# Kernel tuning notes

Measured on AMD Instinct MI355X. Metric: run time of the kernel, lower is better.

## Reference

```python
import jax, jax.numpy as jnp
import numpy as np

NEIGHBORS = 16  # init kwarg 'neighbors'


def _mlp(x, params):
    # SetTransform with reduction='none': pointwise MLP, ReLU between layers, linear output
    for W, b in params[:-1]:
        x = jax.nn.relu(x @ W + b)
    W, b = params[-1]
    return x @ W + b


def setup_inputs() -> dict:
    key = jax.random.key(0)
    B, K, P, DIM, C_IN = 4, 2048, 4096, 3, 64
    C_MID, C_OUT = 32, 128
    WH = 32          # weight_hidden sizes
    FH = 256         # final_hidden size
    FIN = C_IN * C_MID  # 2048, final_conv input

    ks = jax.random.split(key, 16)

    def lin(k, fan_in, fan_out):
        k1, k2 = jax.random.split(k)
        s = 1.0 / np.sqrt(fan_in)
        W = jax.random.uniform(k1, (fan_in, fan_out), minval=-s, maxval=s, dtype=jnp.float32)
        b = jax.random.uniform(k2, (fan_out,), minval=-s, maxval=s, dtype=jnp.float32)
        return W, b

    wc0_W, wc0_b = lin(ks[0], DIM, WH)
    wc1_W, wc1_b = lin(ks[1], WH, WH)
    wc2_W, wc2_b = lin(ks[2], WH, C_MID)
    fc0_W, fc0_b = lin(ks[3], FIN, FH)
    fc1_W, fc1_b = lin(ks[4], FH, C_OUT)

    return {
        "keys": jax.random.normal(ks[5], (B, K, DIM), dtype=jnp.float32),
        "points": jax.random.normal(ks[6], (B, P, DIM), dtype=jnp.float32),
        "feats": jax.random.normal(ks[7], (B, P, C_IN), dtype=jnp.float32),
        "wc0_W": wc0_W, "wc0_b": wc0_b,
        "wc1_W": wc1_W, "wc1_b": wc1_b,
        "wc2_W": wc2_W, "wc2_b": wc2_b,
        "fc0_W": fc0_W, "fc0_b": fc0_b,
        "fc1_W": fc1_W, "fc1_b": fc1_b,
    }


def reference(keys, points, feats,
              wc0_W, wc0_b, wc1_W, wc1_b, wc2_W, wc2_b,
              fc0_W, fc0_b, fc1_W, fc1_b):
    B, K, _ = keys.shape
    # Euclidean dist_fn: rel_pos [B,K,P,dim], squared dist [B,K,P]; all points valid
    dist_vec = points[:, None, :, :] - keys[:, :, None, :]
    dist = jnp.sum(dist_vec * dist_vec, axis=-1)
    # k smallest distances -> neighbor indices [B,K,N]
    _, idxs = jax.lax.top_k(-dist, NEIGHBORS)
    # gather relative positions [B,K,N,dim] and neighbor features [B,K,N,c_in]
    neighbor_rel = jnp.take_along_axis(dist_vec, idxs[..., None], axis=2)
    b_idx = jnp.arange(B)[:, None, None]
    neighbor_feats = feats[b_idx, idxs]
    # per-edge weight MLP: [B,K,N,dim] -> [B,K,N,c_mid]
    m = _mlp(neighbor_rel, [(wc0_W, wc0_b), (wc1_W, wc1_b), (wc2_W, wc2_b)])
    # masked matmul aggregation (all neighbors valid under euclidean dist_fn):
    # m^T @ neighbor_feats -> [B,K,c_mid,c_in], flattened to [B,K,c_mid*c_in]
    e = jnp.einsum('bknm,bknc->bkmc', m, neighbor_feats).reshape(B, K, -1)
    # final pointwise MLP -> [B,K,c_out]
    return _mlp(e, [(fc0_W, fc0_b), (fc1_W, fc1_b)])
```

## Files before the change

### kernel.cpp

```cpp
#include <hip/hip_runtime.h>
#include <cfloat>
#include <climits>

#define BATCH 4
#define KQ    2048
#define NP    4096
#define CIN   64
#define CMID  32
#define NB    16
#define NBINS 4096
#define CANDCAP 256
#define QPB   8

typedef short   bf16x8  __attribute__((ext_vector_type(8)));
typedef float   floatx4 __attribute__((ext_vector_type(4)));

__device__ __forceinline__ unsigned short f2bf(float f) {
  unsigned u = __float_as_uint(f);
  u = (u + 0x7fffu + ((u >> 16) & 1u)) >> 16;
  return (unsigned short)u;
}
__device__ __forceinline__ float bf2f(unsigned short u) {
  return __uint_as_float((unsigned)u << 16);
}

__device__ __forceinline__ void load_lds16(const void* g, void* l) {
  __builtin_amdgcn_global_load_lds(
      (const __attribute__((address_space(1))) unsigned int*)g,
      (__attribute__((address_space(3))) unsigned int*)l, 16, 0, 0);
}

__global__ __launch_bounds__(256) void select_topk(
    const float* __restrict__ keys, const float* __restrict__ points,
    int* __restrict__ nidx_g) {
  __shared__ __align__(16) int hist[NBINS];
  __shared__ int   psum[256];
  __shared__ float cand_d[CANDCAP];
  __shared__ int   cand_i[CANDCAP];
  __shared__ int   nidx[NB];
  __shared__ int   sel_cnt, cand_cnt, sBin, sCbelow;

  const int tid = threadIdx.x;
  const int b   = blockIdx.x >> 11;

#pragma unroll
  for (int t = 0; t < 4; ++t)
    *reinterpret_cast<int4*>(&hist[(tid + t * 256) * 4]) = int4{0, 0, 0, 0};
  if (tid == 0) { sel_cnt = 0; cand_cnt = 0; }

  const float kx = keys[blockIdx.x * 3 + 0];
  const float ky = keys[blockIdx.x * 3 + 1];
  const float kz = keys[blockIdx.x * 3 + 2];
  __syncthreads();

  const float4* pv =
      reinterpret_cast<const float4*>(points + (size_t)b * NP * 3) + (size_t)tid * 12;
  float f[48];
#pragma unroll
  for (int c = 0; c < 12; ++c) {
    const float4 v = pv[c];
    f[c * 4 + 0] = v.x; f[c * 4 + 1] = v.y; f[c * 4 + 2] = v.z; f[c * 4 + 3] = v.w;
  }
  float dreg[16];
#pragma unroll
  for (int j = 0; j < 16; ++j) {
    const float dx = f[j * 3 + 0] - kx;
    const float dy = f[j * 3 + 1] - ky;
    const float dz = f[j * 3 + 2] - kz;
    const float d  = dx * dx + dy * dy + dz * dz;
    dreg[j] = d;
    atomicAdd(&hist[__float_as_uint(d) >> 19], 1);
  }
  __syncthreads();

  {
    const int base = tid * 16;
    int s = 0;
#pragma unroll
    for (int t = 0; t < 4; ++t) {
      const int4 hv = *reinterpret_cast<const int4*>(&hist[base + t * 4]);
      s += hv.x + hv.y + hv.z + hv.w;
    }
    psum[tid] = s;
  }
  __syncthreads();

  if (tid < 64) {
    const int q = psum[tid * 4] + psum[tid * 4 + 1] + psum[tid * 4 + 2] + psum[tid * 4 + 3];
    int incl = q;
#pragma unroll
    for (int off = 1; off < 64; off <<= 1) {
      int u = __shfl_up(incl, off);
      if (tid >= off) incl += u;
    }
    unsigned long long bal = __ballot(incl >= NB);
    int firstlane = __ffsll((long long)bal) - 1;
    if (tid == firstlane) {
      int cum = incl - q;
      int bin = -1;
      for (int t = 0; t < 4 && bin < 0; ++t) {
        const int ps = psum[tid * 4 + t];
        if (cum + ps >= NB) {
          const int b0 = (tid * 4 + t) * 16;
          for (int j = 0; j < 16; ++j) {
            const int h = hist[b0 + j];
            if (cum + h >= NB) { bin = b0 + j; break; }
            cum += h;
          }
        } else cum += ps;
      }
      sBin = bin; sCbelow = cum;
    }
  }
  __syncthreads();

  const unsigned B = (unsigned)sBin;
#pragma unroll
  for (int j = 0; j < 16; ++j) {
    const int i = tid * 16 + j;
    const unsigned bk = __float_as_uint(dreg[j]) >> 19;
    if (bk < B) {
      int pos = atomicAdd(&sel_cnt, 1);
      nidx[pos] = i;
    } else if (bk == B) {
      int pos = atomicAdd(&cand_cnt, 1);
      if (pos < CANDCAP) { cand_d[pos] = dreg[j]; cand_i[pos] = i; }
    }
  }
  __syncthreads();

  {
    const int rem = NB - sCbelow;
    const int cc  = min(cand_cnt, CANDCAP);
    for (int j = tid; j < cc; j += 256) {
      const float dj = cand_d[j]; const int ij = cand_i[j];
      int rank = 0;
      for (int k = 0; k < cc; ++k) {
        const float dk = cand_d[k]; const int ik = cand_i[k];
        rank += (dk < dj || (dk == dj && ik < ij)) ? 1 : 0;
      }
      if (rank < rem) nidx[sCbelow + rank] = ij;
    }
  }
  __syncthreads();

  if (tid < NB) nidx_g[blockIdx.x * NB + tid] = nidx[tid];
}

__global__ __launch_bounds__(256) void edge_prep(
    const float* __restrict__ keys, const float* __restrict__ points,
    const float* __restrict__ feats, const int* __restrict__ nidx_g,
    const float* __restrict__ wc0_W, const float* __restrict__ wc0_b,
    const float* __restrict__ wc1_W, const float* __restrict__ wc1_b,
    const float* __restrict__ wc2_W, const float* __restrict__ wc2_b,
    const float* __restrict__ fc0_W, const float* __restrict__ fc1_W,
    unsigned short* __restrict__ W0T, unsigned short* __restrict__ W1T,
    unsigned short* __restrict__ E) {
  __shared__ __align__(16) float w0[96], b0v[32], w1[1024], b1v[32], w2[1024], b2v[32];
  __shared__ int   idx_s[QPB * NB];
  __shared__ __align__(16) unsigned short m_bf[QPB * NB][40];
  __shared__ __align__(16) char u_mem[128 * 144];
  float (*h2_all)[36]        = reinterpret_cast<float(*)[36]>(u_mem);
  unsigned short (*f_bf)[72] = reinterpret_cast<unsigned short(*)[72]>(u_mem);
  float (*tt)[33]            = reinterpret_cast<float(*)[33]>(u_mem);

  const int tid = threadIdx.x;
  const int bid = blockIdx.x;
  const int q0  = bid * QPB;
  const int b   = q0 >> 11;

  if (bid < 544) {
    const float* W; unsigned short* WT; int K, N, k0, n0;
    if (bid < 512) { W = fc0_W; WT = W0T; K = 2048; N = 256;
                     k0 = (bid >> 3) * 32; n0 = (bid & 7) * 32; }
    else           { W = fc1_W; WT = W1T; K = 256;  N = 128;
                     k0 = ((bid - 512) >> 2) * 32; n0 = ((bid - 512) & 3) * 32; }
    const int tx = tid & 31, ty = tid >> 5;
#pragma unroll
    for (int p = 0; p < 4; ++p)
      tt[ty + p * 8][tx] = W[(size_t)(k0 + ty + p * 8) * N + n0 + tx];
    __syncthreads();
#pragma unroll
    for (int p = 0; p < 4; ++p)
      WT[(size_t)(n0 + ty + p * 8) * K + k0 + tx] = f2bf(tt[tx][ty + p * 8]);
    __syncthreads();
  }

  if (tid < 96) w0[tid] = wc0_W[tid];
  for (int i = tid; i < 1024; i += 256) { w1[i] = wc1_W[i]; w2[i] = wc2_W[i]; }
  if (tid < 32) { b0v[tid] = wc0_b[tid]; b1v[tid] = wc1_b[tid]; b2v[tid] = wc2_b[tid]; }
  if (tid < QPB * NB) idx_s[tid] = nidx_g[q0 * NB + tid];
  __syncthreads();

  const int edge = tid & 127;
  const int half = tid >> 7;
  const int ob   = half * 16;
  const int qe   = edge >> 4;
  const int idx  = idx_s[edge];
  {
    const float* p  = points + ((size_t)b * NP + idx) * 3;
    const float* kq = keys + (size_t)(q0 + qe) * 3;
    const float rx = p[0] - kq[0], ry = p[1] - kq[1], rz = p[2] - kq[2];

    float h1[32];
#pragma unroll
    for (int o4 = 0; o4 < 8; ++o4) {
      const float4 a = *reinterpret_cast<const float4*>(&w0[o4 * 4]);
      const float4 c = *reinterpret_cast<const float4*>(&w0[32 + o4 * 4]);
      const float4 d = *reinterpret_cast<const float4*>(&w0[64 + o4 * 4]);
      const float4 e = *reinterpret_cast<const float4*>(&b0v[o4 * 4]);
      h1[o4 * 4 + 0] = fmaxf(0.f, rx * a.x + ry * c.x + rz * d.x + e.x);
      h1[o4 * 4 + 1] = fmaxf(0.f, rx * a.y + ry * c.y + rz * d.y + e.y);
      h1[o4 * 4 + 2] = fmaxf(0.f, rx * a.z + ry * c.z + rz * d.z + e.z);
      h1[o4 * 4 + 3] = fmaxf(0.f, rx * a.w + ry * c.w + rz * d.w + e.w);
    }

    float acc2[16];
#pragma unroll
    for (int j = 0; j < 16; ++j) acc2[j] = b1v[ob + j];
#pragma unroll
    for (int i = 0; i < 32; ++i) {
      const float hv = h1[i];
#pragma unroll
      for (int j4 = 0; j4 < 4; ++j4) {
        const float4 w = *reinterpret_cast<const float4*>(&w1[i * 32 + ob + j4 * 4]);
        acc2[j4 * 4 + 0] += hv * w.x;
        acc2[j4 * 4 + 1] += hv * w.y;
        acc2[j4 * 4 + 2] += hv * w.z;
        acc2[j4 * 4 + 3] += hv * w.w;
      }
    }
#pragma unroll
    for (int j4 = 0; j4 < 4; ++j4) {
      float4 o4v;
      o4v.x = fmaxf(acc2[j4 * 4 + 0], 0.f);
      o4v.y = fmaxf(acc2[j4 * 4 + 1], 0.f);
      o4v.z = fmaxf(acc2[j4 * 4 + 2], 0.f);
      o4v.w = fmaxf(acc2[j4 * 4 + 3], 0.f);
      *reinterpret_cast<float4*>(&h2_all[edge][ob + j4 * 4]) = o4v;
    }
  }
  __syncthreads();

  float mo[16];
#pragma unroll
  for (int j = 0; j < 16; ++j) mo[j] = b2v[ob + j];
#pragma unroll
  for (int i = 0; i < 32; ++i) {
    const float hv = h2_all[edge][i];
#pragma unroll
    for (int j4 = 0; j4 < 4; ++j4) {
      const float4 w = *reinterpret_cast<const float4*>(&w2[i * 32 + ob + j4 * 4]);
      mo[j4 * 4 + 0] += hv * w.x;
      mo[j4 * 4 + 1] += hv * w.y;
      mo[j4 * 4 + 2] += hv * w.z;
      mo[j4 * 4 + 3] += hv * w.w;
    }
  }
#pragma unroll
  for (int j = 0; j < 8; ++j) {
    const unsigned lo = f2bf(mo[2 * j]), hi = f2bf(mo[2 * j + 1]);
    *reinterpret_cast<unsigned*>(&m_bf[edge][ob + 2 * j]) = lo | (hi << 16);
  }
  __syncthreads();

#pragma unroll
  for (int t = 0; t < 8; ++t) {
    const int task = tid + t * 256;
    const int row = task >> 4, ch = task & 15;
    const float4 v = *reinterpret_cast<const float4*>(
        feats + ((size_t)b * NP + idx_s[row]) * CIN + ch * 4);
    ushort4 o4;
    o4.x = f2bf(v.x); o4.y = f2bf(v.y); o4.z = f2bf(v.z); o4.w = f2bf(v.w);
    *reinterpret_cast<ushort4*>(&f_bf[row][ch * 4]) = o4;
  }
  __syncthreads();

  const int wv = tid >> 6, lane = tid & 63;
  const int co = lane & 7, mg = lane >> 3;
#pragma unroll
  for (int it = 0; it < 2; ++it) {
    const int q = wv + it * 4;
    float acc[4][8] = {};
#pragma unroll
    for (int n = 0; n < 16; ++n) {
      const int row = q * 16 + n;
      const ushort4 m4 = *reinterpret_cast<const ushort4*>(&m_bf[row][mg * 4]);
      const float mv[4] = {bf2f(m4.x), bf2f(m4.y), bf2f(m4.z), bf2f(m4.w)};
      const uint4 fv = *reinterpret_cast<const uint4*>(&f_bf[row][co * 8]);
      float fc[8];
      fc[0] = __uint_as_float(fv.x << 16); fc[1] = __uint_as_float(fv.x & 0xffff0000u);
      fc[2] = __uint_as_float(fv.y << 16); fc[3] = __uint_as_float(fv.y & 0xffff0000u);
      fc[4] = __uint_as_float(fv.z << 16); fc[5] = __uint_as_float(fv.z & 0xffff0000u);
      fc[6] = __uint_as_float(fv.w << 16); fc[7] = __uint_as_float(fv.w & 0xffff0000u);
#pragma unroll
      for (int i = 0; i < 4; ++i)
#pragma unroll
        for (int j = 0; j < 8; ++j) acc[i][j] += mv[i] * fc[j];
    }
    unsigned short* Eq = E + (size_t)(q0 + q) * 2048;
#pragma unroll
    for (int i = 0; i < 4; ++i) {
      const int mid = mg * 4 + i;
      uint4 o;
      o.x = (unsigned)f2bf(acc[i][0]) | ((unsigned)f2bf(acc[i][1]) << 16);
      o.y = (unsigned)f2bf(acc[i][2]) | ((unsigned)f2bf(acc[i][3]) << 16);
      o.z = (unsigned)f2bf(acc[i][4]) | ((unsigned)f2bf(acc[i][5]) << 16);
      o.w = (unsigned)f2bf(acc[i][6]) | ((unsigned)f2bf(acc[i][7]) << 16);
      *reinterpret_cast<uint4*>(&Eq[mid * 64 + co * 8]) = o;
    }
  }
}

template <int KDIM, bool RELU, bool OUTBF16, bool SWIZZLE>
__global__ __launch_bounds__(256) void gemm_mfma(
    const unsigned short* __restrict__ A,
    const unsigned short* __restrict__ Bt,
    const float* __restrict__ bias,
    void* __restrict__ Cout, int ldc) {
  __shared__ __align__(16) unsigned short Al[64 * 128];
  __shared__ __align__(16) unsigned short Bl[64 * 128];
  const int tid  = threadIdx.x;
  int m0, n0;
  if (SWIZZLE) {
    const int L    = blockIdx.x;
    const int slot = L >> 3;
    m0 = ((L & 7) * 16 + (slot >> 2)) * 64;
    n0 = (slot & 3) * 64;
  } else {
    m0 = blockIdx.x * 64;
    n0 = blockIdx.y * 64;
  }
  const int wv   = tid >> 6, lane = tid & 63;
  const int quad = lane >> 4, s = lane & 15;
  const int moff = (wv & 1) * 32, noff = (wv >> 1) * 32;
  const int lr   = lane >> 4;
  const int lc   = lane & 15;

  floatx4 acc[2][2] = {{{0.f,0.f,0.f,0.f},{0.f,0.f,0.f,0.f}},
                       {{0.f,0.f,0.f,0.f},{0.f,0.f,0.f,0.f}}};

  for (int k0 = 0; k0 < KDIM; k0 += 128) {
#pragma unroll
    for (int t = 0; t < 4; ++t) {
      const int R0 = wv * 16 + t * 4;
      const int r  = R0 + lr;
      const int gc = lc ^ (r & 7);
      load_lds16(A  + (size_t)(m0 + r) * KDIM + k0 + gc * 8, &Al[R0 * 128]);
      load_lds16(Bt + (size_t)(n0 + r) * KDIM + k0 + gc * 8, &Bl[R0 * 128]);
    }
    __syncthreads();
#pragma unroll
    for (int h = 0; h < 4; ++h) {
      bf16x8 af[2], bfr[2];
#pragma unroll
      for (int i = 0; i < 2; ++i) {
        const int r = moff + i * 16 + s;
        af[i] = *reinterpret_cast<const bf16x8*>(
            &Al[(size_t)r * 128 + ((((h << 2) | quad) ^ (r & 7)) << 3)]);
      }
#pragma unroll
      for (int j = 0; j < 2; ++j) {
        const int r = noff + j * 16 + s;
        bfr[j] = *reinterpret_cast<const bf16x8*>(
            &Bl[(size_t)r * 128 + ((((h << 2) | quad) ^ (r & 7)) << 3)]);
      }
#pragma unroll
      for (int i = 0; i < 2; ++i)
#pragma unroll
        for (int j = 0; j < 2; ++j)
          acc[i][j] = __builtin_amdgcn_mfma_f32_16x16x32_bf16(af[i], bfr[j], acc[i][j], 0, 0, 0);
    }
    __syncthreads();
  }

#pragma unroll
  for (int i = 0; i < 2; ++i)
#pragma unroll
    for (int j = 0; j < 2; ++j) {
      const int col = n0 + noff + j * 16 + s;
      const float bv = bias[col];
#pragma unroll
      for (int r = 0; r < 4; ++r) {
        const int row = m0 + moff + i * 16 + quad * 4 + r;
        float v = acc[i][j][r] + bv;
        if (RELU) v = fmaxf(v, 0.f);
        if (OUTBF16)
          ((unsigned short*)Cout)[(size_t)row * ldc + col] = f2bf(v);
        else
          ((float*)Cout)[(size_t)row * ldc + col] = v;
      }
    }
}

extern "C" void kernel_launch(void* const* d_in, const int* in_sizes, int n_in,
                              void* d_out, int out_size, void* d_ws, size_t ws_size,
                              hipStream_t stream) {
  const float* keys   = (const float*)d_in[0];
  const float* points = (const float*)d_in[1];
  const float* feats  = (const float*)d_in[2];
  const float* wc0_W  = (const float*)d_in[3];
  const float* wc0_b  = (const float*)d_in[4];
  const float* wc1_W  = (const float*)d_in[5];
  const float* wc1_b  = (const float*)d_in[6];
  const float* wc2_W  = (const float*)d_in[7];
  const float* wc2_b  = (const float*)d_in[8];
  const float* fc0_W  = (const float*)d_in[9];
  const float* fc0_b  = (const float*)d_in[10];
  const float* fc1_W  = (const float*)d_in[11];
  const float* fc1_b  = (const float*)d_in[12];
  float* out = (float*)d_out;

  const int M = BATCH * KQ;
  char* ws = (char*)d_ws;
  unsigned short* E    = (unsigned short*)(ws);
  unsigned short* H16  = (unsigned short*)(ws + (size_t)33554432);
  unsigned short* W0T  = (unsigned short*)(ws + (size_t)37748736);
  unsigned short* W1T  = (unsigned short*)(ws + (size_t)38797312);
  int*            nidx = (int*)(ws + (size_t)38862848);

  select_topk<<<M, 256, 0, stream>>>(keys, points, nidx);
  edge_prep<<<M / QPB, 256, 0, stream>>>(keys, points, feats, nidx,
                                         wc0_W, wc0_b, wc1_W, wc1_b, wc2_W, wc2_b,
                                         fc0_W, fc1_W, W0T, W1T, E);
  gemm_mfma<2048, true,  true,  true ><<<512, 256, 0, stream>>>(E, W0T, fc0_b, H16, 256);
  gemm_mfma<256,  false, false, false><<<dim3(M / 64, 2), 256, 0, stream>>>(H16, W1T, fc1_b, out, 128);
}
```

Baseline: 170.7 us.

## Streamline top-k bin search with per-wave scans and direct global writes

Reworks the threshold-bin search in select_topk. Every wave now computes the histogram prefix scan redundantly with shuffles, using a two-level scan over 64-bin groups and then individual bins. This removes the psum shared array and two block barriers. Selected indices are written straight to global memory instead of staging through shared memory, and the point loads are interleaved with the distance computation to lower register pressure, with launch bounds raised to request higher occupancy. The candidate ranking now runs on one wave only, which can serialize work when many candidates fall in the threshold bin.

```diff
diff --git a/kernel.cpp b/kernel.cpp
--- a/kernel.cpp
+++ b/kernel.cpp
@@ -30,121 +30,111 @@
       (__attribute__((address_space(3))) unsigned int*)l, 16, 0, 0);
 }
 
-__global__ __launch_bounds__(256) void select_topk(
+__global__ __launch_bounds__(256, 8) void select_topk(
     const float* __restrict__ keys, const float* __restrict__ points,
     int* __restrict__ nidx_g) {
   __shared__ __align__(16) int hist[NBINS];
-  __shared__ int   psum[256];
   __shared__ float cand_d[CANDCAP];
   __shared__ int   cand_i[CANDCAP];
-  __shared__ int   nidx[NB];
-  __shared__ int   sel_cnt, cand_cnt, sBin, sCbelow;
-
-  const int tid = threadIdx.x;
-  const int b   = blockIdx.x >> 11;
+  __shared__ int   cnts[2];
+
+  const int tid  = threadIdx.x;
+  const int lane = tid & 63;
+  const int wv   = tid >> 6;
+  const int q    = blockIdx.x;
+  const int b    = q >> 11;
+
+  const float4* pv =
+      reinterpret_cast<const float4*>(points + (size_t)b * NP * 3) + (size_t)tid * 12;
 
 #pragma unroll
   for (int t = 0; t < 4; ++t)
     *reinterpret_cast<int4*>(&hist[(tid + t * 256) * 4]) = int4{0, 0, 0, 0};
-  if (tid == 0) { sel_cnt = 0; cand_cnt = 0; }
-
-  const float kx = keys[blockIdx.x * 3 + 0];
-  const float ky = keys[blockIdx.x * 3 + 1];
-  const float kz = keys[blockIdx.x * 3 + 2];
-  __syncthreads();
-
-  const float4* pv =
-      reinterpret_cast<const float4*>(points + (size_t)b * NP * 3) + (size_t)tid * 12;
-  float f[48];
-#pragma unroll
-  for (int c = 0; c < 12; ++c) {
-    const float4 v = pv[c];
-    f[c * 4 + 0] = v.x; f[c * 4 + 1] = v.y; f[c * 4 + 2] = v.z; f[c * 4 + 3] = v.w;
-  }
+  if (tid < 2) cnts[tid] = 0;
+
+  const float kx = keys[q * 3 + 0];
+  const float ky = keys[q * 3 + 1];
+  const float kz = keys[q * 3 + 2];
+  __syncthreads();
+
   float dreg[16];
 #pragma unroll
-  for (int j = 0; j < 16; ++j) {
-    const float dx = f[j * 3 + 0] - kx;
-    const float dy = f[j * 3 + 1] - ky;
-    const float dz = f[j * 3 + 2] - kz;
-    const float d  = dx * dx + dy * dy + dz * dz;
-    dreg[j] = d;
-    atomicAdd(&hist[__float_as_uint(d) >> 19], 1);
-  }
-  __syncthreads();
-
+  for (int g = 0; g < 4; ++g) {
+    const float4 v0 = pv[g * 3 + 0];
+    const float4 v1 = pv[g * 3 + 1];
+    const float4 v2 = pv[g * 3 + 2];
+    const float px[4] = {v0.x, v0.w, v1.z, v2.y};
+    const float py[4] = {v0.y, v1.x, v1.w, v2.z};
+    const float pz[4] = {v0.z, v1.y, v2.x, v2.w};
+#pragma unroll
+    for (int j = 0; j < 4; ++j) {
+      const float dx = px[j] - kx, dy = py[j] - ky, dz = pz[j] - kz;
+      const float d  = dx * dx + dy * dy + dz * dz;
+      dreg[g * 4 + j] = d;
+      atomicAdd(&hist[__float_as_uint(d) >> 19], 1);
+    }
+  }
+  __syncthreads();
+
+  int s = 0;
   {
-    const int base = tid * 16;
-    int s = 0;
-#pragma unroll
-    for (int t = 0; t < 4; ++t) {
+    const int base = lane * 64;
+#pragma unroll
+    for (int t = 0; t < 16; ++t) {
       const int4 hv = *reinterpret_cast<const int4*>(&hist[base + t * 4]);
       s += hv.x + hv.y + hv.z + hv.w;
     }
-    psum[tid] = s;
-  }
-  __syncthreads();
-
-  if (tid < 64) {
-    const int q = psum[tid * 4] + psum[tid * 4 + 1] + psum[tid * 4 + 2] + psum[tid * 4 + 3];
-    int incl = q;
-#pragma unroll
-    for (int off = 1; off < 64; off <<= 1) {
-      int u = __shfl_up(incl, off);
-      if (tid >= off) incl += u;
-    }
-    unsigned long long bal = __ballot(incl >= NB);
-    int firstlane = __ffsll((long long)bal) - 1;
-    if (tid == firstlane) {
-      int cum = incl - q;
-      int bin = -1;
-      for (int t = 0; t < 4 && bin < 0; ++t) {
-        const int ps = psum[tid * 4 + t];
-        if (cum + ps >= NB) {
-          const int b0 = (tid * 4 + t) * 16;
-          for (int j = 0; j < 16; ++j) {
-            const int h = hist[b0 + j];
-            if (cum + h >= NB) { bin = b0 + j; break; }
-            cum += h;
-          }
-        } else cum += ps;
-      }
-      sBin = bin; sCbelow = cum;
-    }
-  }
-  __syncthreads();
+  }
+  int incl = s;
+#pragma unroll
+  for (int off = 1; off < 64; off <<= 1) {
+    const int u = __shfl_up(incl, off);
+    if (lane >= off) incl += u;
+  }
+  const unsigned long long bal = __ballot(incl >= NB);
+  const int fl = __ffsll((long long)bal) - 1;
+  const int cumBefore = __shfl(incl - s, fl);
+  const int hc = hist[fl * 64 + lane];
+  int incl2 = hc;
+#pragma unroll
+  for (int off = 1; off < 64; off <<= 1) {
+    const int u = __shfl_up(incl2, off);
+    if (lane >= off) incl2 += u;
+  }
+  incl2 += cumBefore;
+  const unsigned long long bal2 = __ballot(incl2 >= NB);
+  const int fl2  = __ffsll((long long)bal2) - 1;
+  const int sBin = fl * 64 + fl2;
+  const int sCb  = __shfl(incl2 - hc, fl2);
 
   const unsigned B = (unsigned)sBin;
+  int* outq = nidx_g + (size_t)q * NB;
 #pragma unroll
   for (int j = 0; j < 16; ++j) {
+    const unsigned bk = __float_as_uint(dreg[j]) >> 19;
     const int i = tid * 16 + j;
-    const unsigned bk = __float_as_uint(dreg[j]) >> 19;
     if (bk < B) {
-      int pos = atomicAdd(&sel_cnt, 1);
-      nidx[pos] = i;
+      outq[atomicAdd(&cnts[0], 1)] = i;
     } else if (bk == B) {
-      int pos = atomicAdd(&cand_cnt, 1);
+      const int pos = atomicAdd(&cnts[1], 1);
       if (pos < CANDCAP) { cand_d[pos] = dreg[j]; cand_i[pos] = i; }
     }
   }
   __syncthreads();
 
-  {
-    const int rem = NB - sCbelow;
-    const int cc  = min(cand_cnt, CANDCAP);
-    for (int j = tid; j < cc; j += 256) {
+  if (wv == 0) {
+    const int rem = NB - sCb;
+    const int cc  = min(cnts[1], CANDCAP);
+    for (int j = lane; j < cc; j += 64) {
       const float dj = cand_d[j]; const int ij = cand_i[j];
       int rank = 0;
       for (int k = 0; k < cc; ++k) {
         const float dk = cand_d[k]; const int ik = cand_i[k];
         rank += (dk < dj || (dk == dj && ik < ij)) ? 1 : 0;
       }
-      if (rank < rem) nidx[sCbelow + rank] = ij;
-    }
-  }
-  __syncthreads();
-
-  if (tid < NB) nidx_g[blockIdx.x * NB + tid] = nidx[tid];
+      if (rank < rem) outq[sCb + rank] = ij;
+    }
+  }
 }
 
 __global__ __launch_bounds__(256) void edge_prep(
```

New measurement: 218.1 us. 27.7% more time.
